# Kernel tuning notes

Hardware: AMD Instinct MI355X
Metric: run time of the kernel (lower is better)

Reference implementation:

```python
import jax, jax.numpy as jnp
import numpy as np

B, N, DIM = 8, 2048, 1024
EPSILON = 0.03
SCALE = 1.0 / np.sqrt(DIM).astype(np.float32)


def setup_inputs() -> dict:
    key = jax.random.key(0)
    ks = jax.random.split(key, 5)
    Q = jax.random.normal(ks[0], (B, N, DIM), dtype=jnp.float32)
    K = jax.random.normal(ks[1], (B, N, DIM), dtype=jnp.float32)
    V = jax.random.normal(ks[2], (B, N, DIM), dtype=jnp.float32)
    # H_net: Linear(dim, dim//2) -> SiLU -> Linear(dim//2, 1); init like torch default scale-ish
    W1 = jax.random.normal(ks[3], (DIM, DIM // 2), dtype=jnp.float32) * (1.0 / np.sqrt(DIM))
    b1 = jnp.zeros((DIM // 2,), dtype=jnp.float32)
    W2 = jax.random.normal(ks[4], (DIM // 2, 1), dtype=jnp.float32) * (1.0 / np.sqrt(DIM // 2))
    b2 = jnp.zeros((1,), dtype=jnp.float32)
    return {"Q": Q, "K": K, "V": V, "W1": W1, "b1": b1, "W2": W2, "b2": b2}


def _mlp(x, W1, b1, W2, b2):
    h = jax.nn.silu(x @ W1 + b1)  # [B,N,dim//2]
    return h @ W2 + b2            # [B,N,1]


def reference(Q, K, V, W1, b1, W2, b2):
    def energy(q, v):
        # scores [B,N,N]
        A = jax.nn.softmax(jnp.einsum('bnd,bmd->bnm', q, K) * SCALE, axis=-1)
        attn_out = jnp.einsum('bnm,bmd->bnd', A, v)
        H = jnp.sum(_mlp(attn_out, W1, b1, W2, b2))
        return H, attn_out

    # grads of scalar energy H w.r.t. Q and V (dH_dV is computed per the
    # original code but discarded by the final split; only dH_dQ survives)
    (dH_dQ, dH_dV), attn_out = jax.grad(energy, argnums=(0, 1), has_aux=True)(Q, V)
    # S_new = cat([Q,V]) + eps*cat([dH_dV, -dH_dQ]); split -> V_new = V - eps*dH_dQ
    V_new = V - EPSILON * dH_dQ
    return V_new + attn_out
```

## Files before the change

### kernel.cpp

```cpp
#include <hip/hip_runtime.h>

typedef __bf16 bf16;
typedef __attribute__((ext_vector_type(8))) __bf16 bf16x8;
typedef __attribute__((ext_vector_type(4))) float f32x4;

#define MEMFENCE asm volatile("" ::: "memory")

__device__ __forceinline__ void gload16(const bf16* g, bf16* l) {
    __builtin_amdgcn_global_load_lds(
        (const __attribute__((address_space(1))) void*)g,
        (__attribute__((address_space(3))) void*)l,
        16, 0, 0);
}

template<int EPI>
__global__ __launch_bounds__(512, 1)
void gemm8p(const bf16* __restrict__ A, const bf16* __restrict__ Bm,
            void* __restrict__ Cp, int Kdim, int lda, int ldb, int ldc,
            long sA, long sB, long sC, float alpha,
            const float* __restrict__ aux1, const bf16* __restrict__ aux3)
{
    __shared__ __align__(16) char smem[163840];

    const int gx = gridDim.x, gy = gridDim.y;
    int lin = blockIdx.x + gx * (blockIdx.y + gy * blockIdx.z);
    const int q = (gx * gy * gridDim.z) >> 3;
    lin = (lin & 7) * q + (lin >> 3);
    const int bx = lin % gx;
    const int rem0 = lin / gx;
    const int by = rem0 % gy;
    const int bz = rem0 / gy;

    const int t0 = threadIdx.x;
    const int w = t0 >> 6, lane = t0 & 63;
    const int wm = w >> 2, wn = w & 3;
    const int m0 = by * 256, n0 = bx * 256;
    const long zb = bz;

    const bf16* Ab = A  + zb * sA + (size_t)m0 * lda;
    const bf16* Bb = Bm + zb * sB + (size_t)n0 * ldb;

    const int sr16 = lane >> 2;
    const int sce  = ((((lane & 3) << 4) ^ (((lane >> 5) & 1) << 5))) >> 1;
    const int r0s = (w >> 1) * 16 + sr16;
    const int c0s = (w & 1) * 32 + sce;
    const bf16* gA0 = Ab + (size_t)r0s * lda + c0s;
    const bf16* gA1 = Ab + (size_t)(128 + r0s) * lda + c0s;
    const bf16* gB0 = Bb + (size_t)r0s * ldb + c0s;
    const bf16* gB1 = Bb + (size_t)(128 + r0s) * ldb + c0s;
    const size_t a64 = (size_t)64 * lda, b64 = (size_t)64 * ldb;
    const int ldsW0 = w * 1024, ldsW1 = (8 + w) * 1024;

    const int lr = lane & 15, lkq = lane >> 4;
    const int phx = ((lane >> 3) & 1) << 5;
    const int frag_base = (lr * 64 + lkq * 16) ^ phx;
    const char* aR = smem + wm * 16384 + frag_base;
    const char* bR = smem + 98304 + (wn >> 1) * 16384 + (wn & 1) * 8192 + frag_base;

    f32x4 acc[8][4] = {};
    const int NTt = Kdim >> 6;

    auto stgA = [&](int h, int u, int off) {
        char* L = smem + off + h * 16384;
        const bf16* g = h ? gA1 : gA0;
        gload16(g + (size_t)u * 64,        (bf16*)(L + ldsW0));
        gload16(g + a64 + (size_t)u * 64,  (bf16*)(L + ldsW1));
    };
    auto stgB = [&](int h, int u, int p) {
        char* L = smem + 98304 + p * 32768 + h * 16384;
        const bf16* g = h ? gB1 : gB0;
        gload16(g + (size_t)u * 64,        (bf16*)(L + ldsW0));
        gload16(g + b64 + (size_t)u * 64,  (bf16*)(L + ldsW1));
    };

    stgA(0, 0, 0);     stgA(1, 0, 0);     stgB(0, 0, 0); stgB(1, 0, 0);
    stgA(0, 1, 32768); stgA(1, 1, 32768); stgB(0, 1, 1); stgB(1, 1, 1);
    asm volatile("s_waitcnt vmcnt(8)" ::: "memory");
    __builtin_amdgcn_s_barrier();
    MEMFENCE;

    bf16x8 a[4][2], b[4][2];

#define QUAD(MFB, NFB)                                                                  \
    __builtin_amdgcn_s_setprio(1);                                                      \
    _Pragma("unroll")                                                                   \
    for (int ks = 0; ks < 2; ++ks)                                                      \
        _Pragma("unroll")                                                               \
        for (int mf = 0; mf < 4; ++mf)                                                  \
            _Pragma("unroll")                                                           \
            for (int nf = 0; nf < 2; ++nf)                                              \
                acc[(MFB) + mf][(NFB) + nf] = __builtin_amdgcn_mfma_f32_16x16x32_bf16(  \
                    a[mf][ks], b[(NFB) + nf][ks], acc[(MFB) + mf][(NFB) + nf], 0, 0, 0);\
    __builtin_amdgcn_s_setprio(0);

    int aOff = 0, sOff = 65536;
    for (int u = 0; u < NTt; ++u) {
        const int p = u & 1;
        const char* aP = aR + aOff;
        const char* bP = bR + p * 32768;
        const bool st2 = (u + 2 < NTt);

        if (st2) stgA(0, u + 2, sOff);
        #pragma unroll
        for (int mf = 0; mf < 4; ++mf)
            #pragma unroll
            for (int ks = 0; ks < 2; ++ks)
                a[mf][ks] = *(const bf16x8*)(aP + (mf * 2 + ks) * 1024);
        #pragma unroll
        for (int nf = 0; nf < 2; ++nf)
            #pragma unroll
            for (int ks = 0; ks < 2; ++ks)
                b[nf][ks] = *(const bf16x8*)(bP + (nf * 2 + ks) * 1024);
        MEMFENCE;
        __builtin_amdgcn_s_barrier();
        QUAD(0, 0)
        MEMFENCE;
        __builtin_amdgcn_s_barrier();

        if (st2) stgA(1, u + 2, sOff);
        #pragma unroll
        for (int nf = 2; nf < 4; ++nf)
            #pragma unroll
            for (int ks = 0; ks < 2; ++ks)
                b[nf][ks] = *(const bf16x8*)(bP + (nf * 2 + ks) * 1024);
        MEMFENCE;
        __builtin_amdgcn_s_barrier();
        QUAD(0, 2)
        MEMFENCE;
        __builtin_amdgcn_s_barrier();

        if (st2) stgB(0, u + 2, p);
        #pragma unroll
        for (int mf = 0; mf < 4; ++mf)
            #pragma unroll
            for (int ks = 0; ks < 2; ++ks)
                a[mf][ks] = *(const bf16x8*)(aP + ((4 + mf) * 2 + ks) * 1024);
        MEMFENCE;
        __builtin_amdgcn_s_barrier();
        QUAD(4, 2)
        MEMFENCE;
        __builtin_amdgcn_s_barrier();

        if (st2) stgB(1, u + 2, p);
        MEMFENCE;
        if (st2) asm volatile("s_waitcnt vmcnt(8)" ::: "memory");
        else     asm volatile("s_waitcnt vmcnt(0)" ::: "memory");
        __builtin_amdgcn_s_barrier();
        QUAD(4, 0)
        MEMFENCE;
        __builtin_amdgcn_s_barrier();
        MEMFENCE;

        aOff = (aOff == 65536) ? 0 : aOff + 32768;
        sOff = (sOff == 65536) ? 0 : sOff + 32768;
    }
#undef QUAD

    const int rb  = m0 + wm * 128 + lkq * 4;
    const int cb0 = n0 + wn * 64 + lr;
    #pragma unroll
    for (int mf = 0; mf < 8; ++mf) {
        #pragma unroll
        for (int r = 0; r < 4; ++r) {
            const int rw = rb + mf * 16 + r;
            float rd = 0.f;
            if (EPI == 1) rd = aux1[zb * 2048 + rw];
            #pragma unroll
            for (int nf = 0; nf < 4; ++nf) {
                const int c = cb0 + nf * 16;
                const size_t ix = (size_t)rw * ldc + c;
                const float v = acc[mf][nf][r];
                if (EPI == 0) {
                    ((bf16*)Cp + zb * sC)[ix] = (bf16)(alpha * v);
                } else if (EPI == 1) {
                    bf16* Cb = (bf16*)Cp + zb * sC;
                    const bf16* Am = aux3 + zb * sC;
                    Cb[ix] = (bf16)((float)Am[ix] * (v - rd));
                } else {
                    float* C = (float*)Cp + zb * sC;
                    const float* Vv = aux1 + zb * sC;
                    const bf16* AOv = aux3 + zb * sC;
                    C[ix] = Vv[ix] + (float)AOv[ix] - alpha * v;
                }
            }
        }
    }
}

template<int EPI, int NF>
__global__ __launch_bounds__(512, 1)
void gemm_nc(const bf16* __restrict__ A, const bf16* __restrict__ Bm,
             void* __restrict__ Cp, int Kdim, int lda, int ldb, int ldc,
             long sA, long sB, long sC, float alpha,
             const float* __restrict__ aux1, const float* __restrict__ aux2,
             const bf16* __restrict__ aux3)
{
    constexpr int SB = NF * 4096;
    __shared__ __align__(16) char smem[65536 + 4 * SB];

    const int gx = gridDim.x, gy = gridDim.y;
    int lin = blockIdx.x + gx * (blockIdx.y + gy * blockIdx.z);
    const int q = (gx * gy * gridDim.z) >> 3;
    lin = (lin & 7) * q + (lin >> 3);
    const int bx = lin % gx;
    const int rem0 = lin / gx;
    const int by = rem0 % gy;
    const int bz = rem0 / gy;

    const int t0 = threadIdx.x;
    const int w = t0 >> 6, lane = t0 & 63;
    const int wm = w >> 2, wn = w & 3;
    const int m0 = by * 256, n0 = bx * (64 * NF);
    const long zb = bz;

    const bf16* Ab = A  + zb * sA + (size_t)m0 * lda;
    const bf16* Bb = Bm + zb * sB + (size_t)n0 * ldb;

    const int sr16 = lane >> 2;
    const int sce  = ((((lane & 3) << 4) ^ (((lane >> 5) & 1) << 5))) >> 1;
    const int stg0 = w * 2, stg1 = w * 2 + 1;
    const bf16* pA0 = Ab + (size_t)(stg0 * 16 + sr16) * lda + sce;
    const bf16* pA1 = Ab + (size_t)(stg1 * 16 + sr16) * lda + sce;
    const bf16* pB0 = Bb + (size_t)((NF == 4 ? stg0 : w) * 16 + sr16) * ldb + sce;
    const bf16* pB1 = Bb + (size_t)(stg1 * 16 + sr16) * ldb + sce;

    const int lr = lane & 15, lkq = lane >> 4;
    const int phx = ((lane >> 3) & 1) << 5;
    const int frag_base = lr * 64 + lkq * 16;

    f32x4 acc[8][NF] = {};
    const int NT = Kdim >> 5;

    auto issueSlot = [&](int p) {
        char* lA = smem + (p & 3) * 16384;
        char* lB = smem + 65536 + (p & 3) * SB;
        const int kt = p << 5;
        gload16(pA0 + kt, (bf16*)(lA + stg0 * 1024));
        gload16(pA1 + kt, (bf16*)(lA + stg1 * 1024));
        if (NF == 4) {
            gload16(pB0 + kt, (bf16*)(lB + stg0 * 1024));
            gload16(pB1 + kt, (bf16*)(lB + stg1 * 1024));
        } else {
            gload16(pB0 + kt, (bf16*)(lB + w * 1024));
        }
    };
    auto rdA = [&](const char* base, int sub) {
        return *(const bf16x8*)(base + (((sub << 10) + frag_base) ^ phx));
    };

    issueSlot(0); issueSlot(1); issueSlot(2);
    if (NF == 4) asm volatile("s_waitcnt vmcnt(4)" ::: "memory");
    else         asm volatile("s_waitcnt vmcnt(3)" ::: "memory");
    __builtin_amdgcn_s_barrier();
    MEMFENCE;

    bf16x8 alo[4], ahi[4], b0[NF], b1[NF];
    {
        const char* cA = smem;
        const char* cB = smem + 65536;
        #pragma unroll
        for (int mf = 0; mf < 4; ++mf) alo[mf] = rdA(cA, wm * 8 + mf);
        #pragma unroll
        for (int nf = 0; nf < NF; ++nf) b0[nf] = rdA(cB, wn * NF + nf);
    }

    auto stepBody = [&](int SL, int s, bf16x8 (&bA)[NF], bf16x8 (&bB)[NF]) {
        if (s + 3 < NT) issueSlot(s + 3);
        const char* cA = smem + SL * 16384;
        #pragma unroll
        for (int mf = 0; mf < 4; ++mf) ahi[mf] = rdA(cA, wm * 8 + 4 + mf);

        __builtin_amdgcn_s_setprio(1);
        #pragma unroll
        for (int mf = 0; mf < 4; ++mf)
            #pragma unroll
            for (int nf = 0; nf < NF; ++nf)
                acc[mf][nf] = __builtin_amdgcn_mfma_f32_16x16x32_bf16(alo[mf], bA[nf], acc[mf][nf], 0, 0, 0);
        __builtin_amdgcn_s_setprio(0);

        if (s + 1 < NT) {
            const int NS = (SL + 1) & 3;
            const char* nA = smem + NS * 16384;
            const char* nB = smem + 65536 + NS * SB;
            #pragma unroll
            for (int mf = 0; mf < 4; ++mf) alo[mf] = rdA(nA, wm * 8 + mf);
            #pragma unroll
            for (int nf = 0; nf < NF; ++nf) bB[nf] = rdA(nB, wn * NF + nf);
        }

        __builtin_amdgcn_s_setprio(1);
        #pragma unroll
        for (int mf = 0; mf < 4; ++mf)
            #pragma unroll
            for (int nf = 0; nf < NF; ++nf)
                acc[4 + mf][nf] = __builtin_amdgcn_mfma_f32_16x16x32_bf16(ahi[mf], bA[nf], acc[4 + mf][nf], 0, 0, 0);
        __builtin_amdgcn_s_setprio(0);

        MEMFENCE;
        if (s + 3 < NT) {
            if (NF == 4) asm volatile("s_waitcnt vmcnt(4)" ::: "memory");
            else         asm volatile("s_waitcnt vmcnt(3)" ::: "memory");
        } else {
            asm volatile("s_waitcnt vmcnt(0)" ::: "memory");
        }
        __builtin_amdgcn_s_barrier();
        MEMFENCE;
    };

    for (int s = 0; s < NT; s += 2) {
        stepBody(s & 3, s, b0, b1);
        stepBody((s + 1) & 3, s + 1, b1, b0);
    }

    const int rb  = m0 + wm * 128 + lkq * 4;
    const int cb0 = n0 + wn * (NF * 16) + lr;
    #pragma unroll
    for (int mf = 0; mf < 8; ++mf) {
        #pragma unroll
        for (int nf = 0; nf < NF; ++nf) {
            const int c = cb0 + nf * 16;
            #pragma unroll
            for (int r = 0; r < 4; ++r) {
                const int rw = rb + mf * 16 + r;
                const size_t ix = (size_t)rw * ldc + c;
                const float v = acc[mf][nf][r];
                if (EPI == 0) {
                    ((bf16*)Cp + zb * sC)[ix] = (bf16)(alpha * v);
                } else {
                    const float u = v + aux1[c];
                    const float sg = 1.f / (1.f + __expf(-u));
                    const float dd = sg * (1.f + u * (1.f - sg));
                    ((bf16*)Cp)[ix] = (bf16)(dd * aux2[c]);
                    ((bf16*)aux3)[ix] = (bf16)v;
                }
            }
        }
    }
}

template<bool DN, bool DT>
__global__ __launch_bounds__(256)
void transcast_k(const float* __restrict__ in, bf16* __restrict__ outN,
                 bf16* __restrict__ outT, int R, int C)
{
    __shared__ float ts[64][65];
    const int t = threadIdx.x;
    const int c0 = blockIdx.x * 64, r0 = blockIdx.y * 64;
    const size_t zoff = (size_t)blockIdx.z * R * C;

    const int rr = t >> 2, cc = (t & 3) * 16;
    float4 f[4];
    const float* src = in + zoff + (size_t)(r0 + rr) * C + c0 + cc;
    #pragma unroll
    for (int i = 0; i < 4; ++i) f[i] = *(const float4*)(src + 4 * i);

    if (DN) {
        bf16x8 h0, h1;
        #pragma unroll
        for (int i = 0; i < 2; ++i) {
            h0[i*4+0] = (bf16)f[i].x;   h0[i*4+1] = (bf16)f[i].y;
            h0[i*4+2] = (bf16)f[i].z;   h0[i*4+3] = (bf16)f[i].w;
            h1[i*4+0] = (bf16)f[i+2].x; h1[i*4+1] = (bf16)f[i+2].y;
            h1[i*4+2] = (bf16)f[i+2].z; h1[i*4+3] = (bf16)f[i+2].w;
        }
        bf16* dst = outN + zoff + (size_t)(r0 + rr) * C + c0 + cc;
        *(bf16x8*)dst = h0;
        *(bf16x8*)(dst + 8) = h1;
    }
    if (DT) {
        #pragma unroll
        for (int i = 0; i < 4; ++i) {
            ts[rr][cc + 4*i + 0] = f[i].x;
            ts[rr][cc + 4*i + 1] = f[i].y;
            ts[rr][cc + 4*i + 2] = f[i].z;
            ts[rr][cc + 4*i + 3] = f[i].w;
        }
        __syncthreads();
        const int ct = t >> 2, rr4 = (t & 3) * 16;
        bf16x8 o0, o1;
        #pragma unroll
        for (int i = 0; i < 8; ++i) o0[i] = (bf16)ts[rr4 + i][ct];
        #pragma unroll
        for (int i = 0; i < 8; ++i) o1[i] = (bf16)ts[rr4 + 8 + i][ct];
        bf16* dst = outT + zoff + (size_t)(c0 + ct) * R + r0 + rr4;
        *(bf16x8*)dst = o0;
        *(bf16x8*)(dst + 8) = o1;
    }
}

__global__ __launch_bounds__(256)
void softmax_k(const bf16* __restrict__ S, bf16* __restrict__ A)
{
    const size_t row = blockIdx.x;
    const int t = threadIdx.x;
    const int wid = t >> 6, lane = t & 63;
    __shared__ float r1[4], r2[4];

    bf16x8 v = *(const bf16x8*)(S + row * 2048 + t * 8);
    float f[8];
    float mx = -1e30f;
    #pragma unroll
    for (int i = 0; i < 8; ++i) { f[i] = (float)v[i]; mx = fmaxf(mx, f[i]); }
    #pragma unroll
    for (int o = 32; o; o >>= 1) mx = fmaxf(mx, __shfl_xor(mx, o, 64));
    if (!lane) r1[wid] = mx;
    __syncthreads();
    mx = fmaxf(fmaxf(r1[0], r1[1]), fmaxf(r1[2], r1[3]));

    float sum = 0.f;
    #pragma unroll
    for (int i = 0; i < 8; ++i) { f[i] = __expf(f[i] - mx); sum += f[i]; }
    #pragma unroll
    for (int o = 32; o; o >>= 1) sum += __shfl_xor(sum, o, 64);
    if (!lane) r2[wid] = sum;
    __syncthreads();
    sum = r2[0] + r2[1] + r2[2] + r2[3];

    const float inv = 1.f / sum;
    bf16x8 ov;
    #pragma unroll
    for (int i = 0; i < 8; ++i) ov[i] = (bf16)(f[i] * inv);
    *(bf16x8*)(A + row * 2048 + t * 8) = ov;
}

__global__ __launch_bounds__(256)
void rowdot_k(const bf16* __restrict__ U, const bf16* __restrict__ H, float* __restrict__ rd)
{
    const int r = blockIdx.x * 4 + (threadIdx.x >> 6);
    const int lane = threadIdx.x & 63;
    bf16x8 uv = *(const bf16x8*)(U + (size_t)r * 512 + lane * 8);
    bf16x8 hv = *(const bf16x8*)(H + (size_t)r * 512 + lane * 8);
    float d = 0.f;
    #pragma unroll
    for (int i = 0; i < 8; ++i) d += (float)uv[i] * (float)hv[i];
    #pragma unroll
    for (int o = 32; o; o >>= 1) d += __shfl_xor(d, o, 64);
    if (!lane) rd[r] = d;
}

extern "C" void kernel_launch(void* const* d_in, const int* in_sizes, int n_in,
                              void* d_out, int out_size, void* d_ws, size_t ws_size,
                              hipStream_t stream)
{
    const float* Q  = (const float*)d_in[0];
    const float* Km = (const float*)d_in[1];
    const float* V  = (const float*)d_in[2];
    const float* W1 = (const float*)d_in[3];
    const float* b1 = (const float*)d_in[4];
    const float* W2 = (const float*)d_in[5];
    float* out = (float*)d_out;

    char* ws = (char*)d_ws;
    bf16* Amat = (bf16*)(ws);
    bf16* AO   = (bf16*)(ws + 67108864);
    bf16* Kb   = AO;
    bf16* KbT  = (bf16*)(ws + 100663296);
    bf16* Vb   = (bf16*)(ws + 134217728);
    bf16* Hb   = Vb;
    bf16* VbT  = (bf16*)(ws + 167772160);
    bf16* U    = VbT;
    bf16* Qb   = (bf16*)(ws + 201326592);
    bf16* VW1b = Qb;
    bf16* W1T  = (bf16*)(ws + 234881024);
    float* rowdot = (float*)(ws + 235929600);
    bf16* S    = (bf16*)d_out;

    const long sQK = 2048L * 1024;
    const long sS  = 2048L * 2048;
    const long sVW = 2048L * 512;
    dim3 blk(256), blkG(512);

    transcast_k<true,  false><<<dim3(16, 32, 8), blk, 0, stream>>>(Q,  Qb, nullptr, 2048, 1024);
    transcast_k<true,  true ><<<dim3(16, 32, 8), blk, 0, stream>>>(Km, Kb, KbT,     2048, 1024);
    transcast_k<true,  true ><<<dim3(16, 32, 8), blk, 0, stream>>>(V,  Vb, VbT,     2048, 1024);
    transcast_k<false, true ><<<dim3(8,  16, 1), blk, 0, stream>>>(W1, nullptr, W1T, 1024, 512);

    gemm8p<0><<<dim3(8, 8, 8), blkG, 0, stream>>>(
        Qb, Kb, S, 1024, 1024, 1024, 2048, sQK, sQK, sS, 0.03125f, nullptr, nullptr);

    gemm_nc<0, 2><<<dim3(4, 8, 8), blkG, 0, stream>>>(
        Vb, W1T, VW1b, 1024, 1024, 1024, 512, sQK, 0, sVW, 1.0f, nullptr, nullptr, nullptr);

    softmax_k<<<dim3(16384), blk, 0, stream>>>(S, Amat);

    gemm8p<0><<<dim3(4, 8, 8), blkG, 0, stream>>>(
        Amat, VbT, AO, 2048, 2048, 2048, 1024, sS, sQK, sQK, 1.0f, nullptr, nullptr);

    gemm_nc<3, 2><<<dim3(4, 64, 1), blkG, 0, stream>>>(
        AO, W1T, U, 1024, 1024, 1024, 512, 0, 0, 0, 1.0f, b1, W2, Hb);

    rowdot_k<<<dim3(4096), blk, 0, stream>>>(U, Hb, rowdot);

    gemm8p<1><<<dim3(8, 8, 8), blkG, 0, stream>>>(
        U, VW1b, Amat, 512, 512, 512, 2048, sVW, sVW, sS, 1.0f, rowdot, Amat);

    gemm8p<2><<<dim3(4, 8, 8), blkG, 0, stream>>>(
        Amat, KbT, out, 2048, 2048, 2048, 1024, sS, sQK, sQK, 0.03f * 0.03125f, V, AO);
}
```

Measured before the change: 436.5 us.

## Restructure GEMM main loop to cut barriers and prefetch next tile fragments

Measured after the change: 420.3 us. 1.04x faster.

```diff
diff --git a/kernel.cpp b/kernel.cpp
--- a/kernel.cpp
+++ b/kernel.cpp
@@ -79,9 +79,19 @@
     __builtin_amdgcn_s_barrier();
     MEMFENCE;
 
-    bf16x8 a[4][2], b[4][2];
-
-#define QUAD(MFB, NFB)                                                                  \
+    bf16x8 a[4][2], bl[2][2], bh[2][2];
+    #pragma unroll
+    for (int mf = 0; mf < 4; ++mf)
+        #pragma unroll
+        for (int ks = 0; ks < 2; ++ks)
+            a[mf][ks] = *(const bf16x8*)(aR + (mf * 2 + ks) * 1024);
+    #pragma unroll
+    for (int nf = 0; nf < 2; ++nf)
+        #pragma unroll
+        for (int ks = 0; ks < 2; ++ks)
+            bh[nf][ks] = *(const bf16x8*)(bR + ((2 + nf) * 2 + ks) * 1024);
+
+#define QUADQ(MFB, NFB, AARR, BARR)                                                     \
     __builtin_amdgcn_s_setprio(1);                                                      \
     _Pragma("unroll")                                                                   \
     for (int ks = 0; ks < 2; ++ks)                                                      \
@@ -90,71 +100,63 @@
             _Pragma("unroll")                                                           \
             for (int nf = 0; nf < 2; ++nf)                                              \
                 acc[(MFB) + mf][(NFB) + nf] = __builtin_amdgcn_mfma_f32_16x16x32_bf16(  \
-                    a[mf][ks], b[(NFB) + nf][ks], acc[(MFB) + mf][(NFB) + nf], 0, 0, 0);\
+                    AARR[mf][ks], BARR[nf][ks], acc[(MFB) + mf][(NFB) + nf], 0, 0, 0);  \
     __builtin_amdgcn_s_setprio(0);
 
-    int aOff = 0, sOff = 65536;
+    int aOff = 0, aOff1 = 32768, sOff = 65536;
     for (int u = 0; u < NTt; ++u) {
         const int p = u & 1;
-        const char* aP = aR + aOff;
-        const char* bP = bR + p * 32768;
-        const bool st2 = (u + 2 < NTt);
+        const char* aP  = aR + aOff;
+        const char* aP1 = aR + aOff1;
+        const char* bP  = bR + p * 32768;
+        const char* bP1 = bR + (p ^ 1) * 32768;
+        const bool st2 = (u + 2 < NTt), nx = (u + 1 < NTt);
 
         if (st2) stgA(0, u + 2, sOff);
         #pragma unroll
-        for (int mf = 0; mf < 4; ++mf)
+        for (int nf = 0; nf < 2; ++nf)
             #pragma unroll
             for (int ks = 0; ks < 2; ++ks)
-                a[mf][ks] = *(const bf16x8*)(aP + (mf * 2 + ks) * 1024);
-        #pragma unroll
-        for (int nf = 0; nf < 2; ++nf)
-            #pragma unroll
-            for (int ks = 0; ks < 2; ++ks)
-                b[nf][ks] = *(const bf16x8*)(bP + (nf * 2 + ks) * 1024);
-        MEMFENCE;
-        __builtin_amdgcn_s_barrier();
-        QUAD(0, 0)
-        MEMFENCE;
-        __builtin_amdgcn_s_barrier();
+                bl[nf][ks] = *(const bf16x8*)(bP + (nf * 2 + ks) * 1024);
+        QUADQ(0, 2, a, bh)
 
         if (st2) stgA(1, u + 2, sOff);
-        #pragma unroll
-        for (int nf = 2; nf < 4; ++nf)
-            #pragma unroll
-            for (int ks = 0; ks < 2; ++ks)
-                b[nf][ks] = *(const bf16x8*)(bP + (nf * 2 + ks) * 1024);
-        MEMFENCE;
-        __builtin_amdgcn_s_barrier();
-        QUAD(0, 2)
-        MEMFENCE;
-        __builtin_amdgcn_s_barrier();
-
-        if (st2) stgB(0, u + 2, p);
+        QUADQ(0, 0, a, bl)
         #pragma unroll
         for (int mf = 0; mf < 4; ++mf)
             #pragma unroll
             for (int ks = 0; ks < 2; ++ks)
                 a[mf][ks] = *(const bf16x8*)(aP + ((4 + mf) * 2 + ks) * 1024);
         MEMFENCE;
+        if (st2)     asm volatile("s_waitcnt vmcnt(4)" ::: "memory");
+        else if (nx) asm volatile("s_waitcnt vmcnt(0)" ::: "memory");
         __builtin_amdgcn_s_barrier();
-        QUAD(4, 2)
         MEMFENCE;
-        __builtin_amdgcn_s_barrier();
+
+        if (st2) stgB(0, u + 2, p);
+        QUADQ(4, 0, a, bl)
 
         if (st2) stgB(1, u + 2, p);
-        MEMFENCE;
-        if (st2) asm volatile("s_waitcnt vmcnt(8)" ::: "memory");
-        else     asm volatile("s_waitcnt vmcnt(0)" ::: "memory");
-        __builtin_amdgcn_s_barrier();
-        QUAD(4, 0)
+        QUADQ(4, 2, a, bh)
+        if (nx) {
+            #pragma unroll
+            for (int mf = 0; mf < 4; ++mf)
+                #pragma unroll
+                for (int ks = 0; ks < 2; ++ks)
+                    a[mf][ks] = *(const bf16x8*)(aP1 + (mf * 2 + ks) * 1024);
+            #pragma unroll
+            for (int nf = 0; nf < 2; ++nf)
+                #pragma unroll
+                for (int ks = 0; ks < 2; ++ks)
+                    bh[nf][ks] = *(const bf16x8*)(bP1 + ((2 + nf) * 2 + ks) * 1024);
+        }
         MEMFENCE;
         __builtin_amdgcn_s_barrier();
         MEMFENCE;
 
-        aOff = (aOff == 65536) ? 0 : aOff + 32768;
-        sOff = (sOff == 65536) ? 0 : sOff + 32768;
-    }
-#undef QUAD
+        const int tmp = aOff; aOff = aOff1; aOff1 = sOff; sOff = tmp;
+    }
+#undef QUADQ
 
     const int rb  = m0 + wm * 128 + lkq * 4;
     const int cb0 = n0 + wn * 64 + lr;
```
